# Performance work log

Measured on AMD Instinct MI355X. Metric: run time of the kernel, lower is better.

Reference implementation:

```python
import jax, jax.numpy as jnp
import numpy as np

N_LAYERS = 3
HIDDEN = 128
N_NODES = 50000
N_EDGES = 800000
NEG_SLOPE = 0.2  # PyG GATConv default negative_slope
EPS = 1e-16      # PyG softmax denominator eps


def setup_inputs() -> dict:
    key = jax.random.key(0)
    ks = jax.random.split(key, 6)
    z = jax.random.normal(ks[0], (N_NODES, HIDDEN), dtype=jnp.float32)
    edge_index = jax.random.randint(ks[1], (2, N_EDGES), 0, N_NODES, dtype=jnp.int32)
    scale = 1.0 / np.sqrt(HIDDEN)
    Ws = jax.random.normal(ks[2], (N_LAYERS, HIDDEN, HIDDEN), dtype=jnp.float32) * scale
    a_src = jax.random.normal(ks[3], (N_LAYERS, HIDDEN), dtype=jnp.float32) * scale
    a_dst = jax.random.normal(ks[4], (N_LAYERS, HIDDEN), dtype=jnp.float32) * scale
    bias = jnp.zeros((N_LAYERS, HIDDEN), dtype=jnp.float32)
    return {"z": z, "edge_index": edge_index, "Ws": Ws, "a_src": a_src,
            "a_dst": a_dst, "bias": bias}


def _gat_conv(h, W, a_s, a_d, b, src, dst):
    # Linear transform: [N, D]
    x = h @ W
    # Per-node attention logits, gathered per edge
    alpha_s = x @ a_s  # [N]
    alpha_d = x @ a_d  # [N]
    e = jax.nn.leaky_relu(alpha_s[src] + alpha_d[dst], NEG_SLOPE)  # [E]
    # Segment softmax over incoming edges of each destination node
    e_max = jax.ops.segment_max(e, dst, num_segments=N_NODES)
    ex = jnp.exp(e - e_max[dst])
    denom = jax.ops.segment_sum(ex, dst, num_segments=N_NODES)
    alpha = ex / (denom[dst] + EPS)  # [E]
    # Weighted scatter-aggregation of source features
    out = jax.ops.segment_sum(x[src] * alpha[:, None], dst, num_segments=N_NODES)
    return out + b


def reference(z, edge_index, Ws, a_src, a_dst, bias):
    # add_self_loops=True (PyG GATConv default)
    loop = jnp.arange(N_NODES, dtype=edge_index.dtype)
    src = jnp.concatenate([edge_index[0], loop])
    dst = jnp.concatenate([edge_index[1], loop])
    h = z
    for l in range(N_LAYERS):
        h = _gat_conv(h, Ws[l], a_src[l], a_dst[l], bias[l], src, dst)
        if l < N_LAYERS - 1:
            h = jax.nn.relu(h)
    return h
```

## Files before the change

### kernel.cpp

```cpp
#include <hip/hip_runtime.h>

#define NN 50000
#define HID 128
#define NE 800000
#define ET (NE + NN)
#define NEG_SLOPE 0.2f
#define CAP 64
#define WTOT (3 * HID * HID)
#define VTOT (3 * 3 * HID)

typedef __attribute__((ext_vector_type(8))) short short8v;
typedef __attribute__((ext_vector_type(4))) float f32x4;

__device__ inline float b2f(unsigned short u) {
    union { unsigned int i; float f; } x; x.i = ((unsigned int)u) << 16; return x.f;
}
__device__ inline float f_lo(unsigned int u) {
    union { unsigned int i; float f; } x; x.i = u << 16; return x.f;
}
__device__ inline float f_hi(unsigned int u) {
    union { unsigned int i; float f; } x; x.i = u & 0xFFFF0000u; return x.f;
}
__device__ inline unsigned short f2b(float f) {
    unsigned int x; __builtin_memcpy(&x, &f, 4);
    unsigned int lsb = (x >> 16) & 1u;
    x += 0x7fffu + lsb;
    return (unsigned short)(x >> 16);
}
__device__ inline void splitbf(float v, unsigned short& hi, unsigned short& lo) {
    hi = f2b(v);
    lo = f2b(v - b2f(hi));
}
__device__ inline float readlane_f(float v, int l) {
    union { float f; int i; } x; x.f = v;
    x.i = __builtin_amdgcn_readlane(x.i, l);
    return x.f;
}

__global__ __launch_bounds__(256) void prep(
        const unsigned short* __restrict__ z, const void* __restrict__ Ws,
        const void* __restrict__ as_, const void* __restrict__ ad_,
        const void* __restrict__ b_, unsigned short* __restrict__ Wb,
        float* __restrict__ asf, float* __restrict__ adf, float* __restrict__ bff,
        int* __restrict__ pos, int* __restrict__ flag) {
    __shared__ int sflag;
    const int t = threadIdx.x;
    if (t < 64) {
        unsigned short a = z[t * 4];
        unsigned short b = z[t * 4 + 2];
        int ea = (a >> 7) & 0xFF, eb = (b >> 7) & 0xFF;
        int w1 = (ea >= 0x9A || (ea <= 0x30 && a != 0)) ? 1 : 0;
        int w2 = (eb >= 0x9A || (eb <= 0x30 && b != 0)) ? 1 : 0;
        int wild = __popcll(__ballot(w1)) + __popcll(__ballot(w2));
        if (t == 0) sflag = (wild < 8) ? 1 : 0;
    }
    __syncthreads();
    const int f = sflag;
    const int gtid = blockIdx.x * 256 + t;
    if (gtid == 0) *flag = f;
    if (gtid < NN) pos[gtid] = 0;
    if (gtid < WTOT) {
        int L = gtid >> 14, k = (gtid >> 7) & 127, n = gtid & 127;
        float v = f ? b2f(((const unsigned short*)Ws)[gtid]) : ((const float*)Ws)[gtid];
        unsigned short hi, lo;
        splitbf(v, hi, lo);
        unsigned short* hbase = Wb + (size_t)L * 2 * HID * HID;
        unsigned short* lbase = hbase + HID * HID;
        int bo = (n * 256 + k * 2) ^ ((n & 7) << 4);
        *(unsigned short*)((char*)hbase + bo) = hi;
        lbase[n * HID + k] = lo;
    } else {
        int i = gtid - WTOT;
        if (i < VTOT) {
            int which = i / (3 * HID), j = i - which * (3 * HID);
            const void* in = which == 0 ? as_ : which == 1 ? ad_ : b_;
            float* o = which == 0 ? asf : which == 1 ? adf : bff;
            o[j] = f ? b2f(((const unsigned short*)in)[j]) : ((const float*)in)[j];
        }
    }
}

#define SCHUNK 1024
__global__ __launch_bounds__(256) void scatter_padded(
        const int* __restrict__ ei, int* __restrict__ pos, int* __restrict__ csr) {
    const int rng  = blockIdx.x & 7;
    const int base = (blockIdx.x >> 3) * SCHUNK;
#pragma unroll
    for (int k = 0; k < SCHUNK / 256; ++k) {
        int e = base + k * 256 + threadIdx.x;
        if (e >= ET) continue;
        int d = (e < NE) ? ei[NE + e] : (e - NE);
        if ((d * 8) / NN != rng) continue;
        int s = (e < NE) ? ei[e] : d;
        int slot = atomicAdd(&pos[d], 1);
        if (slot < CAP) csr[(d << 6) + slot] = s;
    }
}

__global__ __launch_bounds__(256) void gemm_alpha(
        const void* __restrict__ h_, const unsigned short* __restrict__ Wb,
        const float* __restrict__ a_s, const float* __restrict__ a_d,
        unsigned short* __restrict__ x, float* __restrict__ alpha_s, float* __restrict__ alpha_d,
        const int* __restrict__ flag) {
    __shared__ unsigned short Wh[HID * HID];
    const int t = threadIdx.x;
    const int base = blockIdx.x * 64;
    const int hf = *flag;
    const unsigned short* Wlo = Wb + HID * HID;

#pragma unroll
    for (int i = 0; i < 8; ++i) {
        int c = i * 256 + t;
        ((short8v*)Wh)[c] = ((const short8v*)Wb)[c];
    }
    __syncthreads();

    const int w  = t >> 6;
    const int l  = t & 63;
    const int lr = l & 15;
    const int lk = l >> 4;
    const int arow = base + w * 16 + lr;
    const bool rowok = (arow < NN);

    const short8v zv = (short8v){0, 0, 0, 0, 0, 0, 0, 0};
    short8v ahi[4], alo[4];
    if (hf) {
        const unsigned short* hp = (const unsigned short*)h_ + (size_t)arow * HID + lk * 8;
#pragma unroll
        for (int ks = 0; ks < 4; ++ks) {
            ahi[ks] = rowok ? *(const short8v*)(hp + ks * 32) : zv;
            alo[ks] = zv;
        }
    } else {
        const float* hp = (const float*)h_ + (size_t)arow * HID + lk * 8;
#pragma unroll
        for (int ks = 0; ks < 4; ++ks) {
            float4 v0 = make_float4(0.f, 0.f, 0.f, 0.f), v1 = v0;
            if (rowok) {
                v0 = *(const float4*)(hp + ks * 32);
                v1 = *(const float4*)(hp + ks * 32 + 4);
            }
            ushort4 h0, l0, h1, l1;
            splitbf(v0.x, h0.x, l0.x); splitbf(v0.y, h0.y, l0.y);
            splitbf(v0.z, h0.z, l0.z); splitbf(v0.w, h0.w, l0.w);
            splitbf(v1.x, h1.x, l1.x); splitbf(v1.y, h1.y, l1.y);
            splitbf(v1.z, h1.z, l1.z); splitbf(v1.w, h1.w, l1.w);
            ahi[ks] = (short8v){(short)h0.x, (short)h0.y, (short)h0.z, (short)h0.w,
                                (short)h1.x, (short)h1.y, (short)h1.z, (short)h1.w};
            alo[ks] = (short8v){(short)l0.x, (short)l0.y, (short)l0.z, (short)l0.w,
                                (short)l1.x, (short)l1.y, (short)l1.z, (short)l1.w};
        }
    }

    f32x4 acc[8];
#pragma unroll
    for (int nt = 0; nt < 8; ++nt) acc[nt] = (f32x4){0.f, 0.f, 0.f, 0.f};

    if (hf) {
#pragma unroll
        for (int ks = 0; ks < 4; ++ks) {
#pragma unroll
            for (int nt = 0; nt < 8; ++nt) {
                int row = nt * 16 + lr;
                int bo = (row * 256 + ks * 64 + lk * 16) ^ ((lr & 7) << 4);
                short8v bhi = *(const short8v*)((const char*)Wh + bo);
                short8v blo = *(const short8v*)(Wlo + row * HID + ks * 32 + lk * 8);
                acc[nt] = __builtin_amdgcn_mfma_f32_16x16x32_bf16(ahi[ks], bhi, acc[nt], 0, 0, 0);
                acc[nt] = __builtin_amdgcn_mfma_f32_16x16x32_bf16(ahi[ks], blo, acc[nt], 0, 0, 0);
            }
        }
    } else {
#pragma unroll
        for (int ks = 0; ks < 4; ++ks) {
#pragma unroll
            for (int nt = 0; nt < 8; ++nt) {
                int row = nt * 16 + lr;
                int bo = (row * 256 + ks * 64 + lk * 16) ^ ((lr & 7) << 4);
                short8v bhi = *(const short8v*)((const char*)Wh + bo);
                short8v blo = *(const short8v*)(Wlo + row * HID + ks * 32 + lk * 8);
                acc[nt] = __builtin_amdgcn_mfma_f32_16x16x32_bf16(ahi[ks], bhi, acc[nt], 0, 0, 0);
                acc[nt] = __builtin_amdgcn_mfma_f32_16x16x32_bf16(alo[ks], bhi, acc[nt], 0, 0, 0);
                acc[nt] = __builtin_amdgcn_mfma_f32_16x16x32_bf16(ahi[ks], blo, acc[nt], 0, 0, 0);
            }
        }
    }

    float ps[4] = {0.f, 0.f, 0.f, 0.f};
    float pd[4] = {0.f, 0.f, 0.f, 0.f};
#pragma unroll
    for (int nt = 0; nt < 8; ++nt) {
        float asv = a_s[nt * 16 + lr];
        float adv = a_d[nt * 16 + lr];
#pragma unroll
        for (int r = 0; r < 4; ++r) {
            ps[r] = fmaf(acc[nt][r], asv, ps[r]);
            pd[r] = fmaf(acc[nt][r], adv, pd[r]);
        }
    }
#pragma unroll
    for (int m = 8; m >= 1; m >>= 1) {
#pragma unroll
        for (int r = 0; r < 4; ++r) {
            ps[r] += __shfl_xor(ps[r], m, 16);
            pd[r] += __shfl_xor(pd[r], m, 16);
        }
    }
#pragma unroll
    for (int r = 0; r < 4; ++r) {
        int grow = base + w * 16 + lk * 4 + r;
        if (grow < NN) {
#pragma unroll
            for (int nt = 0; nt < 8; ++nt)
                x[(size_t)grow * HID + nt * 16 + lr] = f2b(acc[nt][r]);
            if (lr == 0) { alpha_s[grow] = ps[r]; alpha_d[grow] = pd[r]; }
        }
    }
}

__global__ __launch_bounds__(256) void aggregate_v4(
        const unsigned short* __restrict__ x, const int* __restrict__ deg_,
        const int* __restrict__ csr, const float* __restrict__ als,
        const float* __restrict__ ald, const float* __restrict__ bias,
        void* __restrict__ out, const int* __restrict__ flag, int do_relu) {
    const int node = (blockIdx.x * 256 + threadIdx.x) >> 6;
    const int lane = threadIdx.x & 63;
    if (node >= NN) return;
    const int deg = min(deg_[node], CAP);

    int   sidx = 0;
    float p    = 0.f;
    if (lane < deg) {
        sidx = csr[(node << 6) + lane];
        float e = als[sidx] + ald[node];
        e = fmaxf(e, NEG_SLOPE * e);
        e = fminf(e, 60.f);
        p = __expf(e);
    }
    float den = p;
#pragma unroll
    for (int m = 1; m < 64; m <<= 1) den += __shfl_xor(den, m);
    p *= 1.f / (den + 1e-16f);

    const unsigned int* x2 = (const unsigned int*)x;
    float ax = 0.f, ay = 0.f;
#pragma unroll
    for (int j0 = 0; j0 < CAP; j0 += 16) {
        if (j0 >= deg) break;
        unsigned int u[16]; float pj[16];
#pragma unroll
        for (int k = 0; k < 16; ++k) {
            const int j = j0 + k;
            int ijs = __builtin_amdgcn_readlane(sidx, j);
            pj[k] = readlane_f(p, j);
            const unsigned int* rowp = x2 + (((size_t)(unsigned)ijs) << 6);
            u[k] = rowp[lane];
        }
#pragma unroll
        for (int k = 0; k < 16; ++k) {
            ax = fmaf(pj[k], f_lo(u[k]), ax);
            ay = fmaf(pj[k], f_hi(u[k]), ay);
        }
    }

    float2 bv = ((const float2*)bias)[lane];
    float ox = ax + bv.x;
    float oy = ay + bv.y;
    if (do_relu) { ox = fmaxf(ox, 0.f); oy = fmaxf(oy, 0.f); }
    if (*flag) {
        ushort2 pk; pk.x = f2b(ox); pk.y = f2b(oy);
        *(ushort2*)((unsigned short*)out + (size_t)node * HID + lane * 2) = pk;
    } else {
        ((float2*)out)[(size_t)node * 64 + lane] = make_float2(ox, oy);
    }
}

extern "C" void kernel_launch(void* const* d_in, const int* in_sizes, int n_in,
                              void* d_out, int out_size, void* d_ws, size_t ws_size,
                              hipStream_t stream) {
    const void* z_in  = d_in[0];
    const int*  ei    = (const int*)d_in[1];
    const void* Ws_in = d_in[2];
    const void* as_in = d_in[3];
    const void* ad_in = d_in[4];
    const void* b_in  = d_in[5];

    char* wsp = (char*)d_ws;
    auto alloc = [&](size_t bytes) -> char* {
        char* p = wsp; wsp += (bytes + 255) & ~(size_t)255; return p;
    };
    int*            dflag   = (int*)alloc(4);
    int*            pos     = (int*)alloc(NN * 4);
    int*            csrp    = (int*)alloc((size_t)NN * CAP * 4);
    float*          alpha_s = (float*)alloc(NN * 4);
    float*          alpha_d = (float*)alloc(NN * 4);
    unsigned short* Wb      = (unsigned short*)alloc((size_t)3 * 2 * HID * HID * 2);
    float*          asf     = (float*)alloc(3 * HID * 4);
    float*          adf     = (float*)alloc(3 * HID * 4);
    float*          bff     = (float*)alloc(3 * HID * 4);
    unsigned short* xb      = (unsigned short*)alloc((size_t)NN * HID * 2);

    prep<<<197, 256, 0, stream>>>((const unsigned short*)z_in, Ws_in, as_in, ad_in, b_in,
                                  Wb, asf, adf, bff, pos, dflag);

    const int chunks = (ET + SCHUNK - 1) / SCHUNK;
    scatter_padded<<<chunks * 8, 256, 0, stream>>>(ei, pos, csrp);

    const int gemm_blocks = (NN + 63) / 64;
    const int wave_blocks = (NN + 3) / 4;
    const size_t WL = 2 * HID * HID;

    gemm_alpha<<<gemm_blocks, 256, 0, stream>>>(z_in, Wb, asf, adf, xb, alpha_s, alpha_d, dflag);
    aggregate_v4<<<wave_blocks, 256, 0, stream>>>(xb, pos, csrp, alpha_s, alpha_d, bff, d_out, dflag, 1);

    gemm_alpha<<<gemm_blocks, 256, 0, stream>>>(d_out, Wb + WL, asf + HID, adf + HID,
                                                xb, alpha_s, alpha_d, dflag);
    aggregate_v4<<<wave_blocks, 256, 0, stream>>>(xb, pos, csrp, alpha_s, alpha_d, bff + HID, d_out, dflag, 1);

    gemm_alpha<<<gemm_blocks, 256, 0, stream>>>(d_out, Wb + 2 * WL, asf + 2 * HID,
                                                adf + 2 * HID, xb, alpha_s, alpha_d, dflag);
    aggregate_v4<<<wave_blocks, 256, 0, stream>>>(xb, pos, csrp, alpha_s, alpha_d, bff + 2 * HID, d_out, dflag, 0);
}
```

Baseline: 295.5 us.

## Fuse aggregation with next-layer GEMM and merge scatter with first GEMM

Edge scatter and the first-layer GEMM now run as one launch, with blocks split by index. Each layer's aggregation is fused with the following layer's GEMM: per-block aggregated rows go into LDS as split bf16 hi/lo and feed MFMA directly, so the intermediate hidden tensor never round-trips through global memory. A dedicated final aggregation kernel writes the output, and the dtype flag is now recomputed per kernel instead of stored in memory. The cost is that each wave gathers 16 nodes one after another, and weights are read from global memory rather than LDS. That lowers parallelism in the gather-heavy phase.

After: 314.3 us. 6.4% more time.

```diff
diff --git a/kernel.cpp b/kernel.cpp
--- a/kernel.cpp
+++ b/kernel.cpp
@@ -2,12 +2,17 @@
 
 #define NN 50000
 #define HID 128
+#define HH (HID * HID)
 #define NE 800000
 #define ET (NE + NN)
 #define NEG_SLOPE 0.2f
 #define CAP 64
 #define WTOT (3 * HID * HID)
 #define VTOT (3 * 3 * HID)
+#define SCHUNK 1024
+#define SCAT_VB (((ET + SCHUNK - 1) / SCHUNK) * 8)
+#define GEMM_VB ((NN + 63) / 64)
+#define WL3 (3 * HH)
 
 typedef __attribute__((ext_vector_type(8))) short short8v;
 typedef __attribute__((ext_vector_type(4))) float f32x4;
@@ -36,15 +41,7 @@
     x.i = __builtin_amdgcn_readlane(x.i, l);
     return x.f;
 }
-
-__global__ __launch_bounds__(256) void prep(
-        const unsigned short* __restrict__ z, const void* __restrict__ Ws,
-        const void* __restrict__ as_, const void* __restrict__ ad_,
-        const void* __restrict__ b_, unsigned short* __restrict__ Wb,
-        float* __restrict__ asf, float* __restrict__ adf, float* __restrict__ bff,
-        int* __restrict__ pos, int* __restrict__ flag) {
-    __shared__ int sflag;
-    const int t = threadIdx.x;
+__device__ __forceinline__ int probe_hf_dev(const unsigned short* z, int t, int* sflag) {
     if (t < 64) {
         unsigned short a = z[t * 4];
         unsigned short b = z[t * 4 + 2];
@@ -52,23 +49,33 @@
         int w1 = (ea >= 0x9A || (ea <= 0x30 && a != 0)) ? 1 : 0;
         int w2 = (eb >= 0x9A || (eb <= 0x30 && b != 0)) ? 1 : 0;
         int wild = __popcll(__ballot(w1)) + __popcll(__ballot(w2));
-        if (t == 0) sflag = (wild < 8) ? 1 : 0;
+        if (t == 0) *sflag = (wild < 8) ? 1 : 0;
     }
     __syncthreads();
-    const int f = sflag;
+    return *sflag;
+}
+
+__global__ __launch_bounds__(256) void prep(
+        const unsigned short* __restrict__ z, const void* __restrict__ Ws,
+        const void* __restrict__ as_, const void* __restrict__ ad_,
+        const void* __restrict__ b_, unsigned short* __restrict__ Wb,
+        float* __restrict__ asf, float* __restrict__ adf, float* __restrict__ bff,
+        int* __restrict__ pos) {
+    __shared__ int sflag;
+    const int t = threadIdx.x;
+    const int f = probe_hf_dev(z, t, &sflag);
     const int gtid = blockIdx.x * 256 + t;
-    if (gtid == 0) *flag = f;
     if (gtid < NN) pos[gtid] = 0;
     if (gtid < WTOT) {
         int L = gtid >> 14, k = (gtid >> 7) & 127, n = gtid & 127;
         float v = f ? b2f(((const unsigned short*)Ws)[gtid]) : ((const float*)Ws)[gtid];
         unsigned short hi, lo;
         splitbf(v, hi, lo);
-        unsigned short* hbase = Wb + (size_t)L * 2 * HID * HID;
-        unsigned short* lbase = hbase + HID * HID;
+        unsigned short* hbase = Wb + (size_t)L * WL3;
         int bo = (n * 256 + k * 2) ^ ((n & 7) << 4);
         *(unsigned short*)((char*)hbase + bo) = hi;
-        lbase[n * HID + k] = lo;
+        hbase[HH + n * HID + k]     = lo;
+        hbase[2 * HH + n * HID + k] = hi;
     } else {
         int i = gtid - WTOT;
         if (i < VTOT) {
@@ -80,34 +87,34 @@
     }
 }
 
-#define SCHUNK 1024
-__global__ __launch_bounds__(256) void scatter_padded(
-        const int* __restrict__ ei, int* __restrict__ pos, int* __restrict__ csr) {
-    const int rng  = blockIdx.x & 7;
-    const int base = (blockIdx.x >> 3) * SCHUNK;
-#pragma unroll
-    for (int k = 0; k < SCHUNK / 256; ++k) {
-        int e = base + k * 256 + threadIdx.x;
-        if (e >= ET) continue;
-        int d = (e < NE) ? ei[NE + e] : (e - NE);
-        if ((d * 8) / NN != rng) continue;
-        int s = (e < NE) ? ei[e] : d;
-        int slot = atomicAdd(&pos[d], 1);
-        if (slot < CAP) csr[(d << 6) + slot] = s;
-    }
-}
-
-__global__ __launch_bounds__(256) void gemm_alpha(
-        const void* __restrict__ h_, const unsigned short* __restrict__ Wb,
-        const float* __restrict__ a_s, const float* __restrict__ a_d,
-        unsigned short* __restrict__ x, float* __restrict__ alpha_s, float* __restrict__ alpha_d,
-        const int* __restrict__ flag) {
-    __shared__ unsigned short Wh[HID * HID];
+__global__ __launch_bounds__(256) void scat_gemm0(
+        const unsigned short* __restrict__ z, const int* __restrict__ ei,
+        const unsigned short* __restrict__ Wb, const float* __restrict__ a_s,
+        const float* __restrict__ a_d, int* __restrict__ pos, int* __restrict__ csr,
+        unsigned short* __restrict__ x, float* __restrict__ als, float* __restrict__ ald) {
+    __shared__ unsigned short Wh[HH];
+    __shared__ int sflag;
     const int t = threadIdx.x;
-    const int base = blockIdx.x * 64;
-    const int hf = *flag;
-    const unsigned short* Wlo = Wb + HID * HID;
-
+    const int hf = probe_hf_dev(z, t, &sflag);
+
+    if (blockIdx.x < SCAT_VB) {
+        const int rng  = blockIdx.x & 7;
+        const int base = (blockIdx.x >> 3) * SCHUNK;
+#pragma unroll
+        for (int k = 0; k < SCHUNK / 256; ++k) {
+            int e = base + k * 256 + t;
+            if (e >= ET) continue;
+            int d = (e < NE) ? ei[NE + e] : (e - NE);
+            if ((d * 8) / NN != rng) continue;
+            int s = (e < NE) ? ei[e] : d;
+            int slot = atomicAdd(&pos[d], 1);
+            if (slot < CAP) csr[(d << 6) + slot] = s;
+        }
+        return;
+    }
+
+    const int base = (blockIdx.x - SCAT_VB) * 64;
+    const unsigned short* Wlo = Wb + HH;
 #pragma unroll
     for (int i = 0; i < 8; ++i) {
         int c = i * 256 + t;
@@ -125,14 +132,14 @@
     const short8v zv = (short8v){0, 0, 0, 0, 0, 0, 0, 0};
     short8v ahi[4], alo[4];
     if (hf) {
-        const unsigned short* hp = (const unsigned short*)h_ + (size_t)arow * HID + lk * 8;
+        const unsigned short* hp = z + (size_t)arow * HID + lk * 8;
 #pragma unroll
         for (int ks = 0; ks < 4; ++ks) {
             ahi[ks] = rowok ? *(const short8v*)(hp + ks * 32) : zv;
             alo[ks] = zv;
         }
     } else {
-        const float* hp = (const float*)h_ + (size_t)arow * HID + lk * 8;
+        const float* hp = (const float*)z + (size_t)arow * HID + lk * 8;
 #pragma unroll
         for (int ks = 0; ks < 4; ++ks) {
             float4 v0 = make_float4(0.f, 0.f, 0.f, 0.f), v1 = v0;
@@ -156,32 +163,17 @@
 #pragma unroll
     for (int nt = 0; nt < 8; ++nt) acc[nt] = (f32x4){0.f, 0.f, 0.f, 0.f};
 
-    if (hf) {
-#pragma unroll
-        for (int ks = 0; ks < 4; ++ks) {
-#pragma unroll
-            for (int nt = 0; nt < 8; ++nt) {
-                int row = nt * 16 + lr;
-                int bo = (row * 256 + ks * 64 + lk * 16) ^ ((lr & 7) << 4);
-                short8v bhi = *(const short8v*)((const char*)Wh + bo);
-                short8v blo = *(const short8v*)(Wlo + row * HID + ks * 32 + lk * 8);
-                acc[nt] = __builtin_amdgcn_mfma_f32_16x16x32_bf16(ahi[ks], bhi, acc[nt], 0, 0, 0);
-                acc[nt] = __builtin_amdgcn_mfma_f32_16x16x32_bf16(ahi[ks], blo, acc[nt], 0, 0, 0);
-            }
-        }
-    } else {
-#pragma unroll
-        for (int ks = 0; ks < 4; ++ks) {
-#pragma unroll
-            for (int nt = 0; nt < 8; ++nt) {
-                int row = nt * 16 + lr;
-                int bo = (row * 256 + ks * 64 + lk * 16) ^ ((lr & 7) << 4);
-                short8v bhi = *(const short8v*)((const char*)Wh + bo);
-                short8v blo = *(const short8v*)(Wlo + row * HID + ks * 32 + lk * 8);
-                acc[nt] = __builtin_amdgcn_mfma_f32_16x16x32_bf16(ahi[ks], bhi, acc[nt], 0, 0, 0);
-                acc[nt] = __builtin_amdgcn_mfma_f32_16x16x32_bf16(alo[ks], bhi, acc[nt], 0, 0, 0);
-                acc[nt] = __builtin_amdgcn_mfma_f32_16x16x32_bf16(ahi[ks], blo, acc[nt], 0, 0, 0);
-            }
+#pragma unroll
+    for (int ks = 0; ks < 4; ++ks) {
+#pragma unroll
+        for (int nt = 0; nt < 8; ++nt) {
+            int row = nt * 16 + lr;
+            int bo = (row * 256 + ks * 64 + lk * 16) ^ ((lr & 7) << 4);
+            short8v bhi = *(const short8v*)((const char*)Wh + bo);
+            short8v blo = *(const short8v*)(Wlo + row * HID + ks * 32 + lk * 8);
+            acc[nt] = __builtin_amdgcn_mfma_f32_16x16x32_bf16(ahi[ks], bhi, acc[nt], 0, 0, 0);
+            if (!hf) acc[nt] = __builtin_amdgcn_mfma_f32_16x16x32_bf16(alo[ks], bhi, acc[nt], 0, 0, 0);
+            acc[nt] = __builtin_amdgcn_mfma_f32_16x16x32_bf16(ahi[ks], blo, acc[nt], 0, 0, 0);
         }
     }
 
@@ -212,18 +204,147 @@
 #pragma unroll
             for (int nt = 0; nt < 8; ++nt)
                 x[(size_t)grow * HID + nt * 16 + lr] = f2b(acc[nt][r]);
-            if (lr == 0) { alpha_s[grow] = ps[r]; alpha_d[grow] = pd[r]; }
-        }
-    }
-}
-
-__global__ __launch_bounds__(256) void aggregate_v4(
-        const unsigned short* __restrict__ x, const int* __restrict__ deg_,
-        const int* __restrict__ csr, const float* __restrict__ als,
-        const float* __restrict__ ald, const float* __restrict__ bias,
-        void* __restrict__ out, const int* __restrict__ flag, int do_relu) {
-    const int node = (blockIdx.x * 256 + threadIdx.x) >> 6;
-    const int lane = threadIdx.x & 63;
+            if (lr == 0) { als[grow] = ps[r]; ald[grow] = pd[r]; }
+        }
+    }
+}
+
+__global__ __launch_bounds__(256, 4) void agg_gemm(
+        const unsigned short* __restrict__ xin, const int* __restrict__ deg_,
+        const int* __restrict__ csr, const float* __restrict__ als_in,
+        const float* __restrict__ ald_in, const float* __restrict__ bias,
+        const unsigned short* __restrict__ Whip, const unsigned short* __restrict__ Wlop,
+        const float* __restrict__ a_s, const float* __restrict__ a_d,
+        unsigned short* __restrict__ xout, float* __restrict__ als_out,
+        float* __restrict__ ald_out) {
+    __shared__ unsigned short Ah[64 * HID];
+    __shared__ unsigned short Al[64 * HID];
+    const int t = threadIdx.x;
+    const int base = blockIdx.x * 64;
+    const int w = t >> 6;
+    const int lane = t & 63;
+    const unsigned int* x2 = (const unsigned int*)xin;
+    const float2 bv = ((const float2*)bias)[lane];
+
+    for (int i = 0; i < 16; ++i) {
+        const int node = base + w * 16 + i;
+        const int deg = (node < NN) ? min(deg_[node], CAP) : 0;
+        int   sidx = 0;
+        float p    = 0.f;
+        if (lane < deg) {
+            sidx = csr[(node << 6) + lane];
+            float e = als_in[sidx] + ald_in[node];
+            e = fmaxf(e, NEG_SLOPE * e);
+            e = fminf(e, 60.f);
+            p = __expf(e);
+        }
+        float den = p;
+#pragma unroll
+        for (int m = 1; m < 64; m <<= 1) den += __shfl_xor(den, m);
+        p *= 1.f / (den + 1e-16f);
+
+        float ax = 0.f, ay = 0.f;
+#pragma unroll
+        for (int j0 = 0; j0 < CAP; j0 += 16) {
+            if (j0 >= deg) break;
+            unsigned int u[16]; float pj[16];
+#pragma unroll
+            for (int k = 0; k < 16; ++k) {
+                const int j = j0 + k;
+                int ijs = __builtin_amdgcn_readlane(sidx, j);
+                pj[k] = readlane_f(p, j);
+                const unsigned int* rowp = x2 + (((size_t)(unsigned)ijs) << 6);
+                u[k] = rowp[lane];
+            }
+#pragma unroll
+            for (int k = 0; k < 16; ++k) {
+                ax = fmaf(pj[k], f_lo(u[k]), ax);
+                ay = fmaf(pj[k], f_hi(u[k]), ay);
+            }
+        }
+        float ox = fmaxf(ax + bv.x, 0.f);
+        float oy = fmaxf(ay + bv.y, 0.f);
+        unsigned short hx, lx, hy, ly;
+        splitbf(ox, hx, lx); splitbf(oy, hy, ly);
+        const int r = w * 16 + i;
+        const int bo = (r * 256 + lane * 4) ^ ((r & 7) << 4);
+        ushort2 ph; ph.x = hx; ph.y = hy;
+        ushort2 pl; pl.x = lx; pl.y = ly;
+        *(ushort2*)((char*)Ah + bo) = ph;
+        *(ushort2*)((char*)Al + bo) = pl;
+    }
+    __syncthreads();
+
+    const int lr = lane & 15;
+    const int lk = lane >> 4;
+    const int ar = w * 16 + lr;
+    short8v ahi[4], alo[4];
+#pragma unroll
+    for (int ks = 0; ks < 4; ++ks) {
+        int ab = (ar * 256 + ks * 64 + lk * 16) ^ ((ar & 7) << 4);
+        ahi[ks] = *(const short8v*)((const char*)Ah + ab);
+        alo[ks] = *(const short8v*)((const char*)Al + ab);
+    }
+
+    f32x4 acc[8];
+#pragma unroll
+    for (int nt = 0; nt < 8; ++nt) acc[nt] = (f32x4){0.f, 0.f, 0.f, 0.f};
+
+#pragma unroll
+    for (int ks = 0; ks < 4; ++ks) {
+#pragma unroll
+        for (int nt = 0; nt < 8; ++nt) {
+            int row = nt * 16 + lr;
+            short8v bhi = *(const short8v*)(Whip + row * HID + ks * 32 + lk * 8);
+            short8v blo = *(const short8v*)(Wlop + row * HID + ks * 32 + lk * 8);
+            acc[nt] = __builtin_amdgcn_mfma_f32_16x16x32_bf16(ahi[ks], bhi, acc[nt], 0, 0, 0);
+            acc[nt] = __builtin_amdgcn_mfma_f32_16x16x32_bf16(alo[ks], bhi, acc[nt], 0, 0, 0);
+            acc[nt] = __builtin_amdgcn_mfma_f32_16x16x32_bf16(ahi[ks], blo, acc[nt], 0, 0, 0);
+        }
+    }
+
+    float ps[4] = {0.f, 0.f, 0.f, 0.f};
+    float pd[4] = {0.f, 0.f, 0.f, 0.f};
+#pragma unroll
+    for (int nt = 0; nt < 8; ++nt) {
+        float asv = a_s[nt * 16 + lr];
+        float adv = a_d[nt * 16 + lr];
+#pragma unroll
+        for (int r = 0; r < 4; ++r) {
+            ps[r] = fmaf(acc[nt][r], asv, ps[r]);
+            pd[r] = fmaf(acc[nt][r], adv, pd[r]);
+        }
+    }
+#pragma unroll
+    for (int m = 8; m >= 1; m >>= 1) {
+#pragma unroll
+        for (int r = 0; r < 4; ++r) {
+            ps[r] += __shfl_xor(ps[r], m, 16);
+            pd[r] += __shfl_xor(pd[r], m, 16);
+        }
+    }
+#pragma unroll
+    for (int r = 0; r < 4; ++r) {
+        int grow = base + w * 16 + lk * 4 + r;
+        if (grow < NN) {
+#pragma unroll
+            for (int nt = 0; nt < 8; ++nt)
+                xout[(size_t)grow * HID + nt * 16 + lr] = f2b(acc[nt][r]);
+            if (lr == 0) { als_out[grow] = ps[r]; ald_out[grow] = pd[r]; }
+        }
+    }
+}
+
+__global__ __launch_bounds__(256) void agg_fin(
+        const unsigned short* __restrict__ z, const unsigned short* __restrict__ x,
+        const int* __restrict__ deg_, const int* __restrict__ csr,
+        const float* __restrict__ als, const float* __restrict__ ald,
+        const float* __restrict__ bias, void* __restrict__ out) {
+    __shared__ int sflag;
+    const int t = threadIdx.x;
+    const int hf = probe_hf_dev(z, t, &sflag);
+    const int node = (blockIdx.x * 256 + t) >> 6;
+    const int lane = t & 63;
     if (node >= NN) return;
     const int deg = min(deg_[node], CAP);
 
@@ -265,8 +386,7 @@
     float2 bv = ((const float2*)bias)[lane];
     float ox = ax + bv.x;
     float oy = ay + bv.y;
-    if (do_relu) { ox = fmaxf(ox, 0.f); oy = fmaxf(oy, 0.f); }
-    if (*flag) {
+    if (hf) {
         ushort2 pk; pk.x = f2b(ox); pk.y = f2b(oy);
         *(ushort2*)((unsigned short*)out + (size_t)node * HID + lane * 2) = pk;
     } else {
@@ -277,46 +397,43 @@
 extern "C" void kernel_launch(void* const* d_in, const int* in_sizes, int n_in,
                               void* d_out, int out_size, void* d_ws, size_t ws_size,
                               hipStream_t stream) {
-    const void* z_in  = d_in[0];
-    const int*  ei    = (const int*)d_in[1];
-    const void* Ws_in = d_in[2];
-    const void* as_in = d_in[3];
-    const void* ad_in = d_in[4];
-    const void* b_in  = d_in[5];
+    const unsigned short* z  = (const unsigned short*)d_in[0];
+    const int*            ei = (const int*)d_in[1];
+    const void*           Ws = d_in[2];
+    const void*           as = d_in[3];
+    const void*           ad = d_in[4];
+    const void*           bb = d_in[5];
 
     char* wsp = (char*)d_ws;
     auto alloc = [&](size_t bytes) -> char* {
         char* p = wsp; wsp += (bytes + 255) & ~(size_t)255; return p;
     };
-    int*            dflag   = (int*)alloc(4);
-    int*            pos     = (int*)alloc(NN * 4);
-    int*            csrp    = (int*)alloc((size_t)NN * CAP * 4);
-    float*          alpha_s = (float*)alloc(NN * 4);
-    float*          alpha_d = (float*)alloc(NN * 4);
-    unsigned short* Wb      = (unsigned short*)alloc((size_t)3 * 2 * HID * HID * 2);
-    float*          asf     = (float*)alloc(3 * HID * 4);
-    float*          adf     = (float*)alloc(3 * HID * 4);
-    float*          bff     = (float*)alloc(3 * HID * 4);
-    unsigned short* xb      = (unsigned short*)alloc((size_t)NN * HID * 2);
-
-    prep<<<197, 256, 0, stream>>>((const unsigned short*)z_in, Ws_in, as_in, ad_in, b_in,
-                                  Wb, asf, adf, bff, pos, dflag);
-
-    const int chunks = (ET + SCHUNK - 1) / SCHUNK;
-    scatter_padded<<<chunks * 8, 256, 0, stream>>>(ei, pos, csrp);
-
-    const int gemm_blocks = (NN + 63) / 64;
-    const int wave_blocks = (NN + 3) / 4;
-    const size_t WL = 2 * HID * HID;
-
-    gemm_alpha<<<gemm_blocks, 256, 0, stream>>>(z_in, Wb, asf, adf, xb, alpha_s, alpha_d, dflag);
-    aggregate_v4<<<wave_blocks, 256, 0, stream>>>(xb, pos, csrp, alpha_s, alpha_d, bff, d_out, dflag, 1);
-
-    gemm_alpha<<<gemm_blocks, 256, 0, stream>>>(d_out, Wb + WL, asf + HID, adf + HID,
-                                                xb, alpha_s, alpha_d, dflag);
-    aggregate_v4<<<wave_blocks, 256, 0, stream>>>(xb, pos, csrp, alpha_s, alpha_d, bff + HID, d_out, dflag, 1);
-
-    gemm_alpha<<<gemm_blocks, 256, 0, stream>>>(d_out, Wb + 2 * WL, asf + 2 * HID,
-                                                adf + 2 * HID, xb, alpha_s, alpha_d, dflag);
-    aggregate_v4<<<wave_blocks, 256, 0, stream>>>(xb, pos, csrp, alpha_s, alpha_d, bff + 2 * HID, d_out, dflag, 0);
-}
+    int*            pos  = (int*)alloc(NN * 4);
+    int*            csrp = (int*)alloc((size_t)NN * CAP * 4);
+    float*          alsA = (float*)alloc(NN * 4);
+    float*          aldA = (float*)alloc(NN * 4);
+    float*          alsB = (float*)alloc(NN * 4);
+    float*          aldB = (float*)alloc(NN * 4);
+    unsigned short* Wb   = (unsigned short*)alloc((size_t)3 * WL3 * 2);
+    float*          asf  = (float*)alloc(3 * HID * 4);
+    float*          adf  = (float*)alloc(3 * HID * 4);
+    float*          bff  = (float*)alloc(3 * HID * 4);
+    unsigned short* xb0  = (unsigned short*)alloc((size_t)NN * HID * 2);
+    unsigned short* xb1  = (unsigned short*)alloc((size_t)NN * HID * 2);
+
+    prep<<<197, 256, 0, stream>>>(z, Ws, as, ad, bb, Wb, asf, adf, bff, pos);
+
+    scat_gemm0<<<SCAT_VB + GEMM_VB, 256, 0, stream>>>(z, ei, Wb, asf, adf,
+                                                      pos, csrp, xb0, alsA, aldA);
+
+    agg_gemm<<<GEMM_VB, 256, 0, stream>>>(xb0, pos, csrp, alsA, aldA, bff,
+                                          Wb + WL3 + 2 * HH, Wb + WL3 + HH,
+                                          asf + HID, adf + HID, xb1, alsB, aldB);
+
+    agg_gemm<<<GEMM_VB, 256, 0, stream>>>(xb1, pos, csrp, alsB, aldB, bff + HID,
+                                          Wb + 2 * WL3 + 2 * HH, Wb + 2 * WL3 + HH,
+                                          asf + 2 * HID, adf + 2 * HID, xb0, alsA, aldA);
+
+    agg_fin<<<(NN + 3) / 4, 256, 0, stream>>>(z, xb0, pos, csrp, alsA, aldA,
+                                              bff + 2 * HID, d_out);
+}
```
